# Performance work log

Hardware: AMD Instinct MI355X
Metric: run time of the kernel (lower is better)

Reference implementation:

```python
import jax, jax.numpy as jnp
from jax import lax
import numpy as np

B, S, H = 4, 4096, 1024
NH, HD, L = 8, 128, 64
EPS = 1e-8


def setup_inputs() -> dict:
    key = jax.random.key(0)
    ks = jax.random.split(key, 11)
    std = 0.02
    d = NH * HD
    return {
        "f_in": jax.random.normal(ks[0], (B, S, H), jnp.float32),
        "i_in": jax.random.normal(ks[1], (B, S, H), jnp.float32),
        "z_in": jax.random.normal(ks[2], (B, S, H), jnp.float32),
        "o_in": jax.random.normal(ks[3], (B, S, H), jnp.float32),
        "c0": jax.random.normal(ks[4], (B, NH, HD), jnp.float32),
        "h0": jax.random.normal(ks[5], (B, NH, HD), jnp.float32),
        "Wf": jax.random.normal(ks[6], (d, H), jnp.float32) * std,
        "bf": jnp.zeros((d,), jnp.float32),
        "Wi": jax.random.normal(ks[7], (d, H), jnp.float32) * std,
        "bi": jnp.zeros((d,), jnp.float32),
        "Wz": jax.random.normal(ks[8], (d, H), jnp.float32) * std,
        "bz": jnp.zeros((d,), jnp.float32),
        "Wo": jax.random.normal(ks[9], (d, H), jnp.float32) * std,
        "bo": jnp.zeros((d,), jnp.float32),
        "Wp": jax.random.normal(ks[10], (H, d), jnp.float32) * std,
        "bp": jnp.zeros((H,), jnp.float32),
    }


def _to_blocks(x):
    # (B,S,NH*HD) -> (n_blocks, B, NH, HD, L)
    nb = S // L
    return x.reshape(B, nb, L, NH, HD).transpose(1, 0, 3, 4, 2)


def reference(f_in, i_in, z_in, o_in, c0, h0, Wf, bf, Wi, bi, Wz, bz, Wo, bo, Wp, bp):
    fx = _to_blocks(f_in @ Wf.T + bf)
    ix = _to_blocks(i_in @ Wi.T + bi)
    zx = _to_blocks(z_in @ Wz.T + bz)
    ox = _to_blocks(o_in @ Wo.T + bo)

    f = jax.nn.sigmoid(fx + 1.0)            # (nb,B,NH,HD,L)
    o = jax.nn.sigmoid(ox)
    upd = jax.nn.sigmoid(ix) * jnp.tanh(zx)

    k = jnp.arange(L)[:, None]
    l = jnp.arange(L + 1)[None, :]
    ones_mask = l >= k + 1                   # set to 1 before cumulative log-prod
    zeros_mask = l >= k + 2                  # strictly-future entries zeroed

    def block_step(c, blk):
        fb, ub, ob = blk                     # each (B,NH,HD,L)
        cf = jnp.concatenate(
            [fb, jnp.ones(fb.shape[:3] + (1,), fb.dtype)], axis=3)  # (B,NH,HD,L+1)
        Fm = jnp.broadcast_to(cf[:, :, :, None, :], fb.shape[:3] + (L, L + 1))
        Fm = jnp.where(ones_mask, 1.0, Fm)
        # reverse cumulative product in log space (matches torch eps trick)
        Fm = jnp.exp(jnp.flip(jnp.cumsum(jnp.flip(jnp.log(Fm + EPS), -1), -1), -1)) - EPS
        Fm = jnp.where(zeros_mask, 0.0, Fm)  # (B,NH,HD,L,L+1)
        u = jnp.concatenate([c[..., None], ub], axis=3)  # (B,NH,HD,L+1)
        cs = jnp.einsum('bhdkl,bhdl->bhdk', Fm, u)       # (B,NH,HD,L)
        hs = ob * jnp.tanh(cs)
        return cs[..., -1], hs

    last_c, hs = lax.scan(block_step, c0, (f, upd, o))   # hs: (nb,B,NH,HD,L)
    last_h = hs[-1][..., -1]
    y = hs.transpose(1, 0, 4, 2, 3).reshape(B, S, NH * HD)
    y = y @ Wp.T + bp                                    # (B,S,H)
    return y, last_c, last_h
```

## Files before the change

kernel.cpp:

```cpp
#include <hip/hip_runtime.h>
#include <hip/hip_bf16.h>
#include <type_traits>

#define GATE_ELEMS 16777216ull
#define W_ELEMS    1048576ull

typedef float f32x4 __attribute__((ext_vector_type(4)));
typedef short s16x8 __attribute__((ext_vector_type(8)));
typedef unsigned short u16;

__device__ __forceinline__ u16 f2bf(float f) {
  union { float f; unsigned u; } v; v.f = f;
  unsigned r = v.u + 0x7fffu + ((v.u >> 16) & 1u);
  return (u16)(r >> 16);
}
__device__ __forceinline__ float bf2f(u16 u) {
  union { unsigned u; float f; } v; v.u = ((unsigned)u) << 16;
  return v.f;
}
__device__ __forceinline__ float sigmoidf_(float x) {
  return 1.0f / (1.0f + __expf(-x));
}
__device__ __forceinline__ float tanhf_(float x) {
  x = fminf(fmaxf(x, -15.f), 15.f);
  const float e = __expf(2.f * x);
  return (e - 1.f) / (e + 1.f);
}

__device__ __forceinline__ void load_lds16(const u16* g, u16* l) {
  __builtin_amdgcn_global_load_lds(
      (const __attribute__((address_space(1))) unsigned int*)g,
      (__attribute__((address_space(3))) unsigned int*)l, 16, 0, 0);
}

__global__ void cvt_x_kernel(const float* __restrict__ x0, const float* __restrict__ x1,
                             const float* __restrict__ x2, const float* __restrict__ x3,
                             u16* __restrict__ dst) {
  const float* src = (blockIdx.y == 0) ? x0 : (blockIdx.y == 1) ? x1
                   : (blockIdx.y == 2) ? x2 : x3;
  u16* d = dst + (size_t)blockIdx.y * GATE_ELEMS;
  const size_t i = ((size_t)blockIdx.x * 256 + threadIdx.x) * 8;
  const float4 a = *reinterpret_cast<const float4*>(src + i);
  const float4 b = *reinterpret_cast<const float4*>(src + i + 4);
  ushort4 lo = make_ushort4(f2bf(a.x), f2bf(a.y), f2bf(a.z), f2bf(a.w));
  ushort4 hi = make_ushort4(f2bf(b.x), f2bf(b.y), f2bf(b.z), f2bf(b.w));
  *reinterpret_cast<ushort4*>(d + i)     = lo;
  *reinterpret_cast<ushort4*>(d + i + 4) = hi;
}

__global__ void cvt_w_kernel(const float* __restrict__ w0, const float* __restrict__ w1,
                             const float* __restrict__ w2, const float* __restrict__ w3,
                             const float* __restrict__ w4, u16* __restrict__ dst) {
  const float* src = (blockIdx.y == 0) ? w0 : (blockIdx.y == 1) ? w1
                   : (blockIdx.y == 2) ? w2 : (blockIdx.y == 3) ? w3 : w4;
  u16* d = dst + (size_t)blockIdx.y * W_ELEMS;
  const size_t i = ((size_t)blockIdx.x * 256 + threadIdx.x) * 8;
  const float4 a = *reinterpret_cast<const float4*>(src + i);
  const float4 b = *reinterpret_cast<const float4*>(src + i + 4);
  ushort4 lo = make_ushort4(f2bf(a.x), f2bf(a.y), f2bf(a.z), f2bf(a.w));
  ushort4 hi = make_ushort4(f2bf(b.x), f2bf(b.y), f2bf(b.z), f2bf(b.w));
  *reinterpret_cast<ushort4*>(d + i)     = lo;
  *reinterpret_cast<ushort4*>(d + i + 4) = hi;
}

template <typename OT>
__global__ __launch_bounds__(256, 3)
void gemm_bt_bf16(const u16* __restrict__ A, const u16* __restrict__ B,
                  const float* __restrict__ bias, OT* __restrict__ C,
                  int M, int N, int K) {
  __shared__ __align__(16) u16 As[128 * 32];
  __shared__ __align__(16) u16 Bs[128 * 32];
  const int tid  = threadIdx.x;
  const int lane = tid & 63;
  const int wave = tid >> 6;
  const int wr = wave >> 1;
  const int wc = wave & 1;

  const int cpx = gridDim.x >> 3;
  int bid = blockIdx.x;
  bid = (bid & 7) * cpx + (bid >> 3);
  const int nbx = N >> 7;
  const int m0 = (bid / nbx) * 128;
  const int n0 = (bid % nbx) * 128;

  f32x4 acc[4][4];
#pragma unroll
  for (int i = 0; i < 4; ++i)
#pragma unroll
    for (int j = 0; j < 4; ++j)
      acc[i][j] = (f32x4){0.f, 0.f, 0.f, 0.f};

  const int frow = lane & 15;
  const int kq   = lane >> 4;
  const int krow = kq * 8;

  const int lrow = lane >> 2;
  const int lcol = (lane & 3) * 8;

  for (int kt = 0; kt < K; kt += 32) {
#pragma unroll
    for (int i = 0; i < 2; ++i) {
      const int rb = (i * 4 + wave) * 16;
      load_lds16(A + (size_t)(m0 + rb + lrow) * K + kt + lcol, &As[rb * 32]);
      load_lds16(B + (size_t)(n0 + rb + lrow) * K + kt + lcol, &Bs[rb * 32]);
    }
    __syncthreads();

    s16x8 afr[4], bfr[4];
#pragma unroll
    for (int mf = 0; mf < 4; ++mf)
      afr[mf] = *reinterpret_cast<const s16x8*>(&As[(wr * 64 + mf * 16 + frow) * 32 + krow]);
#pragma unroll
    for (int nf = 0; nf < 4; ++nf)
      bfr[nf] = *reinterpret_cast<const s16x8*>(&Bs[(wc * 64 + nf * 16 + frow) * 32 + krow]);
#pragma unroll
    for (int mf = 0; mf < 4; ++mf)
#pragma unroll
      for (int nf = 0; nf < 4; ++nf)
        acc[mf][nf] = __builtin_amdgcn_mfma_f32_16x16x32_bf16(afr[mf], bfr[nf], acc[mf][nf], 0, 0, 0);
    __syncthreads();
  }

#pragma unroll
  for (int nf = 0; nf < 4; ++nf) {
    const int col = n0 + wc * 64 + nf * 16 + frow;
    const float bv = bias[col];
#pragma unroll
    for (int mf = 0; mf < 4; ++mf) {
      const int rbase = m0 + wr * 64 + mf * 16 + kq * 4;
#pragma unroll
      for (int r = 0; r < 4; ++r) {
        const float v = acc[mf][nf][r] + bv;
        if constexpr (std::is_same<OT, float>::value)
          C[(size_t)(rbase + r) * N + col] = v;
        else
          C[(size_t)(rbase + r) * N + col] = f2bf(v);
      }
    }
  }
}

__global__ void scan_pass1(const u16* __restrict__ fx, const u16* __restrict__ ix,
                           const u16* __restrict__ zx,
                           float* __restrict__ P, float* __restrict__ cl) {
  const int t  = blockIdx.x * 256 + threadIdx.x;
  const int jg = (t & 255) * 4;
  const int q  = (t >> 8) & 63;
  const int b  = t >> 14;
  const size_t base = ((size_t)(b * 4096 + q * 64)) * 1024 + jg;
  float Pp[4] = {1.f, 1.f, 1.f, 1.f};
  float c[4]  = {0.f, 0.f, 0.f, 0.f};
  for (int s = 0; s < 64; ++s) {
    const size_t o = base + (size_t)s * 1024;
    const ushort4 fv = *reinterpret_cast<const ushort4*>(fx + o);
    const ushort4 iv = *reinterpret_cast<const ushort4*>(ix + o);
    const ushort4 zv = *reinterpret_cast<const ushort4*>(zx + o);
    const u16* fp = (const u16*)&fv;
    const u16* ip = (const u16*)&iv;
    const u16* zp = (const u16*)&zv;
#pragma unroll
    for (int k = 0; k < 4; ++k) {
      const float f = sigmoidf_(bf2f(fp[k]) + 1.f);
      const float u = sigmoidf_(bf2f(ip[k])) * tanhf_(bf2f(zp[k]));
      Pp[k] *= f;
      c[k] = f * c[k] + u;
    }
  }
  const int sidx = q * 4096 + b * 1024 + jg;
  *reinterpret_cast<float4*>(P + sidx)  = make_float4(Pp[0], Pp[1], Pp[2], Pp[3]);
  *reinterpret_cast<float4*>(cl + sidx) = make_float4(c[0], c[1], c[2], c[3]);
}

__global__ void scan_pass2(const float* __restrict__ P, const float* __restrict__ cl,
                           const float* __restrict__ c0, float* __restrict__ cin,
                           float* __restrict__ lastc) {
  const int idx = blockIdx.x * 256 + threadIdx.x;
  float carry = c0[idx];
#pragma unroll
  for (int q = 0; q < 64; ++q) {
    const int s = q * 4096 + idx;
    cin[s] = carry;
    carry = fmaf(P[s], carry, cl[s]);
  }
  lastc[idx] = carry;
}

__global__ void scan_pass3(const u16* __restrict__ fx, const u16* __restrict__ ix,
                           const u16* __restrict__ zx, const u16* __restrict__ ox,
                           const float* __restrict__ cin,
                           u16* __restrict__ h, float* __restrict__ lasth) {
  const int t  = blockIdx.x * 256 + threadIdx.x;
  const int jg = (t & 255) * 4;
  const int q  = (t >> 8) & 63;
  const int b  = t >> 14;
  const size_t base = ((size_t)(b * 4096 + q * 64)) * 1024 + jg;
  const float4 ci = *reinterpret_cast<const float4*>(cin + q * 4096 + b * 1024 + jg);
  float c[4]  = {ci.x, ci.y, ci.z, ci.w};
  float hv[4] = {0.f, 0.f, 0.f, 0.f};
  for (int s = 0; s < 64; ++s) {
    const size_t o = base + (size_t)s * 1024;
    const ushort4 fv = *reinterpret_cast<const ushort4*>(fx + o);
    const ushort4 iv = *reinterpret_cast<const ushort4*>(ix + o);
    const ushort4 zv = *reinterpret_cast<const ushort4*>(zx + o);
    const ushort4 ov = *reinterpret_cast<const ushort4*>(ox + o);
    const u16* fp = (const u16*)&fv;
    const u16* ip = (const u16*)&iv;
    const u16* zp = (const u16*)&zv;
    const u16* op = (const u16*)&ov;
    ushort4 hw;
    u16* hp = (u16*)&hw;
#pragma unroll
    for (int k = 0; k < 4; ++k) {
      const float f = sigmoidf_(bf2f(fp[k]) + 1.f);
      const float u = sigmoidf_(bf2f(ip[k])) * tanhf_(bf2f(zp[k]));
      c[k] = f * c[k] + u;
      hv[k] = sigmoidf_(bf2f(op[k])) * tanhf_(c[k]);
      hp[k] = f2bf(hv[k]);
    }
    *reinterpret_cast<ushort4*>(h + o) = hw;
  }
  if (q == 63)
    *reinterpret_cast<float4*>(lasth + b * 1024 + jg) =
        make_float4(hv[0], hv[1], hv[2], hv[3]);
}

extern "C" void kernel_launch(void* const* d_in, const int* in_sizes, int n_in,
                              void* d_out, int out_size, void* d_ws, size_t ws_size,
                              hipStream_t stream) {
  const float* xin[4]  = {(const float*)d_in[0], (const float*)d_in[1],
                          (const float*)d_in[2], (const float*)d_in[3]};
  const float* c0      = (const float*)d_in[4];
  const float* W[5]    = {(const float*)d_in[6], (const float*)d_in[8],
                          (const float*)d_in[10], (const float*)d_in[12],
                          (const float*)d_in[14]};
  const float* bias[5] = {(const float*)d_in[7], (const float*)d_in[9],
                          (const float*)d_in[11], (const float*)d_in[13],
                          (const float*)d_in[15]};
  float* out = (float*)d_out;

  u16* xbf = (u16*)d_ws;
  u16* wbf = xbf + 4 * GATE_ELEMS;
  float* Pbuf   = (float*)(wbf + 5 * W_ELEMS);
  float* clbuf  = Pbuf + 262144;
  float* cinbuf = clbuf + 262144;

  u16* gp[4];
  gp[0] = (u16*)d_out;
  gp[1] = xbf;
  gp[2] = xbf + GATE_ELEMS;
  gp[3] = xbf + 2 * GATE_ELEMS;
  u16* h = xbf + 3 * GATE_ELEMS;

  cvt_x_kernel<<<dim3(8192, 4), 256, 0, stream>>>(xin[0], xin[1], xin[2], xin[3], xbf);
  cvt_w_kernel<<<dim3(512, 5), 256, 0, stream>>>(W[0], W[1], W[2], W[3], W[4], wbf);

  const dim3 gg(1024, 1, 1);
  for (int g = 0; g < 4; ++g)
    gemm_bt_bf16<u16><<<gg, 256, 0, stream>>>(
        xbf + (size_t)g * GATE_ELEMS, wbf + (size_t)g * W_ELEMS, bias[g],
        gp[g], 16384, 1024, 1024);

  scan_pass1<<<256, 256, 0, stream>>>(gp[0], gp[1], gp[2], Pbuf, clbuf);
  scan_pass2<<<16, 256, 0, stream>>>(Pbuf, clbuf, c0, cinbuf, out + GATE_ELEMS);
  scan_pass3<<<256, 256, 0, stream>>>(gp[0], gp[1], gp[2], gp[3], cinbuf, h,
                                      out + GATE_ELEMS + 4096);

  gemm_bt_bf16<float><<<gg, 256, 0, stream>>>(h, wbf + 4 * W_ELEMS, bias[4],
                                              out, 16384, 1024, 1024);
}
```

Measured before the change: 671.1 us.

## Replace GEMM with 256x256-tile, 4-stage async-LDS pipelined bf16 kernel

Replaces the 128x128 single-buffered GEMM with a 256x256 tile kernel using 512 threads and a four-slot LDS ring buffer (128 KB dynamic shared memory). Global-to-LDS loads for tile k+3 are issued while MFMAs run on tile k, with explicit vmcnt waits, barriers and setprio to overlap memory with compute. The aim is to hide load latency and raise operand reuse per block. The x-conversion kernel also handles 16 elements per thread with 16-byte stores. Risks are lower occupancy from the large LDS footprint and fragile hand-tuned waitcnt logic.

```diff
diff --git a/kernel.cpp b/kernel.cpp
--- a/kernel.cpp
+++ b/kernel.cpp
@@ -39,13 +39,18 @@
   const float* src = (blockIdx.y == 0) ? x0 : (blockIdx.y == 1) ? x1
                    : (blockIdx.y == 2) ? x2 : x3;
   u16* d = dst + (size_t)blockIdx.y * GATE_ELEMS;
-  const size_t i = ((size_t)blockIdx.x * 256 + threadIdx.x) * 8;
-  const float4 a = *reinterpret_cast<const float4*>(src + i);
-  const float4 b = *reinterpret_cast<const float4*>(src + i + 4);
-  ushort4 lo = make_ushort4(f2bf(a.x), f2bf(a.y), f2bf(a.z), f2bf(a.w));
-  ushort4 hi = make_ushort4(f2bf(b.x), f2bf(b.y), f2bf(b.z), f2bf(b.w));
-  *reinterpret_cast<ushort4*>(d + i)     = lo;
-  *reinterpret_cast<ushort4*>(d + i + 4) = hi;
+  const size_t i = ((size_t)blockIdx.x * 256 + threadIdx.x) * 16;
+#pragma unroll
+  for (int half = 0; half < 2; ++half) {
+    const float4 a = *reinterpret_cast<const float4*>(src + i + half * 8);
+    const float4 b = *reinterpret_cast<const float4*>(src + i + half * 8 + 4);
+    s16x8 w;
+    w[0] = (short)f2bf(a.x); w[1] = (short)f2bf(a.y);
+    w[2] = (short)f2bf(a.z); w[3] = (short)f2bf(a.w);
+    w[4] = (short)f2bf(b.x); w[5] = (short)f2bf(b.y);
+    w[6] = (short)f2bf(b.z); w[7] = (short)f2bf(b.w);
+    *reinterpret_cast<s16x8*>(d + i + half * 8) = w;
+  }
 }
 
 __global__ void cvt_w_kernel(const float* __restrict__ w0, const float* __restrict__ w1,
@@ -57,84 +62,154 @@
   const size_t i = ((size_t)blockIdx.x * 256 + threadIdx.x) * 8;
   const float4 a = *reinterpret_cast<const float4*>(src + i);
   const float4 b = *reinterpret_cast<const float4*>(src + i + 4);
-  ushort4 lo = make_ushort4(f2bf(a.x), f2bf(a.y), f2bf(a.z), f2bf(a.w));
-  ushort4 hi = make_ushort4(f2bf(b.x), f2bf(b.y), f2bf(b.z), f2bf(b.w));
-  *reinterpret_cast<ushort4*>(d + i)     = lo;
-  *reinterpret_cast<ushort4*>(d + i + 4) = hi;
+  s16x8 w;
+  w[0] = (short)f2bf(a.x); w[1] = (short)f2bf(a.y);
+  w[2] = (short)f2bf(a.z); w[3] = (short)f2bf(a.w);
+  w[4] = (short)f2bf(b.x); w[5] = (short)f2bf(b.y);
+  w[6] = (short)f2bf(b.z); w[7] = (short)f2bf(b.w);
+  *reinterpret_cast<s16x8*>(d + i) = w;
+}
+
+__device__ __forceinline__ void stage_half(
+    const u16* __restrict__ A, const u16* __restrict__ B,
+    int m0, int n0, int kt, int hp, u16* lds, int tid) {
+  const u16* mat = (hp < 2) ? A : B;
+  const int gr0 = ((hp < 2) ? m0 : n0) + (hp & 1) * 128;
+  const int o   = tid * 16;
+  const int row = o >> 6;
+  const int col = (o & 63) >> 1;
+  const int slot = ((kt & 3) * 4 + hp) * 4096;
+  load_lds16(mat + (size_t)(gr0 + row) * 1024 + kt * 32 + col,
+             lds + slot + (tid >> 6) * 512);
 }
 
 template <typename OT>
-__global__ __launch_bounds__(256, 3)
-void gemm_bt_bf16(const u16* __restrict__ A, const u16* __restrict__ B,
-                  const float* __restrict__ bias, OT* __restrict__ C,
-                  int M, int N, int K) {
-  __shared__ __align__(16) u16 As[128 * 32];
-  __shared__ __align__(16) u16 Bs[128 * 32];
+__global__ __launch_bounds__(512, 2)
+void gemm_256(const u16* __restrict__ A, const u16* __restrict__ B,
+              const float* __restrict__ bias, OT* __restrict__ C) {
+  extern __shared__ u16 lds[];
   const int tid  = threadIdx.x;
   const int lane = tid & 63;
   const int wave = tid >> 6;
-  const int wr = wave >> 1;
-  const int wc = wave & 1;
-
-  const int cpx = gridDim.x >> 3;
+  const int wm = wave >> 2;
+  const int wn = wave & 3;
+  const int frow = lane & 15;
+  const int kq   = lane >> 4;
+
   int bid = blockIdx.x;
-  bid = (bid & 7) * cpx + (bid >> 3);
-  const int nbx = N >> 7;
-  const int m0 = (bid / nbx) * 128;
-  const int n0 = (bid % nbx) * 128;
-
-  f32x4 acc[4][4];
-#pragma unroll
-  for (int i = 0; i < 4; ++i)
+  bid = (bid & 7) * 32 + (bid >> 3);
+  const int m0 = (bid >> 2) * 256;
+  const int n0 = (bid & 3) * 256;
+
+  f32x4 acc[8][4];
+#pragma unroll
+  for (int i = 0; i < 8; ++i)
 #pragma unroll
     for (int j = 0; j < 4; ++j)
       acc[i][j] = (f32x4){0.f, 0.f, 0.f, 0.f};
 
-  const int frow = lane & 15;
-  const int kq   = lane >> 4;
-  const int krow = kq * 8;
-
-  const int lrow = lane >> 2;
-  const int lcol = (lane & 3) * 8;
-
-  for (int kt = 0; kt < K; kt += 32) {
-#pragma unroll
-    for (int i = 0; i < 2; ++i) {
-      const int rb = (i * 4 + wave) * 16;
-      load_lds16(A + (size_t)(m0 + rb + lrow) * K + kt + lcol, &As[rb * 32]);
-      load_lds16(B + (size_t)(n0 + rb + lrow) * K + kt + lcol, &Bs[rb * 32]);
-    }
-    __syncthreads();
-
-    s16x8 afr[4], bfr[4];
-#pragma unroll
-    for (int mf = 0; mf < 4; ++mf)
-      afr[mf] = *reinterpret_cast<const s16x8*>(&As[(wr * 64 + mf * 16 + frow) * 32 + krow]);
-#pragma unroll
-    for (int nf = 0; nf < 4; ++nf)
-      bfr[nf] = *reinterpret_cast<const s16x8*>(&Bs[(wc * 64 + nf * 16 + frow) * 32 + krow]);
-#pragma unroll
-    for (int mf = 0; mf < 4; ++mf)
-#pragma unroll
-      for (int nf = 0; nf < 4; ++nf)
-        acc[mf][nf] = __builtin_amdgcn_mfma_f32_16x16x32_bf16(afr[mf], bfr[nf], acc[mf][nf], 0, 0, 0);
-    __syncthreads();
+#pragma unroll
+  for (int k = 0; k < 3; ++k)
+#pragma unroll
+    for (int hp = 0; hp < 4; ++hp)
+      stage_half(A, B, m0, n0, k, hp, lds, tid);
+  asm volatile("s_waitcnt vmcnt(8)" ::: "memory");
+  __builtin_amdgcn_s_barrier();
+
+  const int rb = (wn & 1) * 64;
+
+#pragma unroll 4
+  for (int kt = 0; kt < 32; ++kt) {
+    const int slotbase = (kt & 3) * 4;
+    const u16* Ar = lds + (slotbase + wm) * 4096;
+    const u16* Br = lds + (slotbase + 2 + (wn >> 1)) * 4096;
+
+    s16x8 a0 = *reinterpret_cast<const s16x8*>(&Ar[(0 * 16 + frow) * 32 + kq * 8]);
+    s16x8 a1 = *reinterpret_cast<const s16x8*>(&Ar[(1 * 16 + frow) * 32 + kq * 8]);
+    s16x8 a2 = *reinterpret_cast<const s16x8*>(&Ar[(2 * 16 + frow) * 32 + kq * 8]);
+    s16x8 a3 = *reinterpret_cast<const s16x8*>(&Ar[(3 * 16 + frow) * 32 + kq * 8]);
+    s16x8 b0 = *reinterpret_cast<const s16x8*>(&Br[(rb + 0 * 16 + frow) * 32 + kq * 8]);
+    s16x8 b1 = *reinterpret_cast<const s16x8*>(&Br[(rb + 1 * 16 + frow) * 32 + kq * 8]);
+    s16x8 b2 = *reinterpret_cast<const s16x8*>(&Br[(rb + 2 * 16 + frow) * 32 + kq * 8]);
+    s16x8 b3 = *reinterpret_cast<const s16x8*>(&Br[(rb + 3 * 16 + frow) * 32 + kq * 8]);
+    if (kt <= 28) {
+      stage_half(A, B, m0, n0, kt + 3, 0, lds, tid);
+      stage_half(A, B, m0, n0, kt + 3, 1, lds, tid);
+    }
+    __builtin_amdgcn_s_barrier();
+    asm volatile("s_waitcnt lgkmcnt(0)" ::: "memory");
+    __builtin_amdgcn_sched_barrier(0);
+    __builtin_amdgcn_s_setprio(1);
+    acc[0][0] = __builtin_amdgcn_mfma_f32_16x16x32_bf16(a0, b0, acc[0][0], 0, 0, 0);
+    acc[0][1] = __builtin_amdgcn_mfma_f32_16x16x32_bf16(a0, b1, acc[0][1], 0, 0, 0);
+    acc[0][2] = __builtin_amdgcn_mfma_f32_16x16x32_bf16(a0, b2, acc[0][2], 0, 0, 0);
+    acc[0][3] = __builtin_amdgcn_mfma_f32_16x16x32_bf16(a0, b3, acc[0][3], 0, 0, 0);
+    acc[1][0] = __builtin_amdgcn_mfma_f32_16x16x32_bf16(a1, b0, acc[1][0], 0, 0, 0);
+    acc[1][1] = __builtin_amdgcn_mfma_f32_16x16x32_bf16(a1, b1, acc[1][1], 0, 0, 0);
+    acc[1][2] = __builtin_amdgcn_mfma_f32_16x16x32_bf16(a1, b2, acc[1][2], 0, 0, 0);
+    acc[1][3] = __builtin_amdgcn_mfma_f32_16x16x32_bf16(a1, b3, acc[1][3], 0, 0, 0);
+    acc[2][0] = __builtin_amdgcn_mfma_f32_16x16x32_bf16(a2, b0, acc[2][0], 0, 0, 0);
+    acc[2][1] = __builtin_amdgcn_mfma_f32_16x16x32_bf16(a2, b1, acc[2][1], 0, 0, 0);
+    acc[2][2] = __builtin_amdgcn_mfma_f32_16x16x32_bf16(a2, b2, acc[2][2], 0, 0, 0);
+    acc[2][3] = __builtin_amdgcn_mfma_f32_16x16x32_bf16(a2, b3, acc[2][3], 0, 0, 0);
+    acc[3][0] = __builtin_amdgcn_mfma_f32_16x16x32_bf16(a3, b0, acc[3][0], 0, 0, 0);
+    acc[3][1] = __builtin_amdgcn_mfma_f32_16x16x32_bf16(a3, b1, acc[3][1], 0, 0, 0);
+    acc[3][2] = __builtin_amdgcn_mfma_f32_16x16x32_bf16(a3, b2, acc[3][2], 0, 0, 0);
+    acc[3][3] = __builtin_amdgcn_mfma_f32_16x16x32_bf16(a3, b3, acc[3][3], 0, 0, 0);
+    __builtin_amdgcn_s_setprio(0);
+    __builtin_amdgcn_sched_barrier(0);
+    __builtin_amdgcn_s_barrier();
+
+    a0 = *reinterpret_cast<const s16x8*>(&Ar[(4 * 16 + frow) * 32 + kq * 8]);
+    a1 = *reinterpret_cast<const s16x8*>(&Ar[(5 * 16 + frow) * 32 + kq * 8]);
+    a2 = *reinterpret_cast<const s16x8*>(&Ar[(6 * 16 + frow) * 32 + kq * 8]);
+    a3 = *reinterpret_cast<const s16x8*>(&Ar[(7 * 16 + frow) * 32 + kq * 8]);
+    if (kt <= 28) {
+      stage_half(A, B, m0, n0, kt + 3, 2, lds, tid);
+      stage_half(A, B, m0, n0, kt + 3, 3, lds, tid);
+    }
+    __builtin_amdgcn_s_barrier();
+    asm volatile("s_waitcnt lgkmcnt(0)" ::: "memory");
+    __builtin_amdgcn_sched_barrier(0);
+    __builtin_amdgcn_s_setprio(1);
+    acc[4][0] = __builtin_amdgcn_mfma_f32_16x16x32_bf16(a0, b0, acc[4][0], 0, 0, 0);
+    acc[4][1] = __builtin_amdgcn_mfma_f32_16x16x32_bf16(a0, b1, acc[4][1], 0, 0, 0);
+    acc[4][2] = __builtin_amdgcn_mfma_f32_16x16x32_bf16(a0, b2, acc[4][2], 0, 0, 0);
+    acc[4][3] = __builtin_amdgcn_mfma_f32_16x16x32_bf16(a0, b3, acc[4][3], 0, 0, 0);
+    acc[5][0] = __builtin_amdgcn_mfma_f32_16x16x32_bf16(a1, b0, acc[5][0], 0, 0, 0);
+    acc[5][1] = __builtin_amdgcn_mfma_f32_16x16x32_bf16(a1, b1, acc[5][1], 0, 0, 0);
+    acc[5][2] = __builtin_amdgcn_mfma_f32_16x16x32_bf16(a1, b2, acc[5][2], 0, 0, 0);
+    acc[5][3] = __builtin_amdgcn_mfma_f32_16x16x32_bf16(a1, b3, acc[5][3], 0, 0, 0);
+    acc[6][0] = __builtin_amdgcn_mfma_f32_16x16x32_bf16(a2, b0, acc[6][0], 0, 0, 0);
+    acc[6][1] = __builtin_amdgcn_mfma_f32_16x16x32_bf16(a2, b1, acc[6][1], 0, 0, 0);
+    acc[6][2] = __builtin_amdgcn_mfma_f32_16x16x32_bf16(a2, b2, acc[6][2], 0, 0, 0);
+    acc[6][3] = __builtin_amdgcn_mfma_f32_16x16x32_bf16(a2, b3, acc[6][3], 0, 0, 0);
+    acc[7][0] = __builtin_amdgcn_mfma_f32_16x16x32_bf16(a3, b0, acc[7][0], 0, 0, 0);
+    acc[7][1] = __builtin_amdgcn_mfma_f32_16x16x32_bf16(a3, b1, acc[7][1], 0, 0, 0);
+    acc[7][2] = __builtin_amdgcn_mfma_f32_16x16x32_bf16(a3, b2, acc[7][2], 0, 0, 0);
+    acc[7][3] = __builtin_amdgcn_mfma_f32_16x16x32_bf16(a3, b3, acc[7][3], 0, 0, 0);
+    __builtin_amdgcn_s_setprio(0);
+    __builtin_amdgcn_sched_barrier(0);
+    if (kt <= 28)      asm volatile("s_waitcnt vmcnt(8)" ::: "memory");
+    else if (kt == 29) asm volatile("s_waitcnt vmcnt(4)" ::: "memory");
+    else if (kt == 30) asm volatile("s_waitcnt vmcnt(0)" ::: "memory");
+    __builtin_amdgcn_s_barrier();
   }
 
 #pragma unroll
   for (int nf = 0; nf < 4; ++nf) {
-    const int col = n0 + wc * 64 + nf * 16 + frow;
+    const int col = n0 + wn * 64 + nf * 16 + frow;
     const float bv = bias[col];
 #pragma unroll
-    for (int mf = 0; mf < 4; ++mf) {
-      const int rbase = m0 + wr * 64 + mf * 16 + kq * 4;
+    for (int mf = 0; mf < 8; ++mf) {
+      const int rbase = m0 + wm * 128 + mf * 16 + kq * 4;
 #pragma unroll
       for (int r = 0; r < 4; ++r) {
         const float v = acc[mf][nf][r] + bv;
         if constexpr (std::is_same<OT, float>::value)
-          C[(size_t)(rbase + r) * N + col] = v;
+          C[(size_t)(rbase + r) * 1024 + col] = v;
         else
-          C[(size_t)(rbase + r) * N + col] = f2bf(v);
+          C[(size_t)(rbase + r) * 1024 + col] = f2bf(v);
       }
     }
   }
@@ -238,6 +313,11 @@
                           (const float*)d_in[15]};
   float* out = (float*)d_out;
 
+  (void)hipFuncSetAttribute((const void*)gemm_256<u16>,
+                            hipFuncAttributeMaxDynamicSharedMemorySize, 131072);
+  (void)hipFuncSetAttribute((const void*)gemm_256<float>,
+                            hipFuncAttributeMaxDynamicSharedMemorySize, 131072);
+
   u16* xbf = (u16*)d_ws;
   u16* wbf = xbf + 4 * GATE_ELEMS;
   float* Pbuf   = (float*)(wbf + 5 * W_ELEMS);
@@ -251,20 +331,17 @@
   gp[3] = xbf + 2 * GATE_ELEMS;
   u16* h = xbf + 3 * GATE_ELEMS;
 
-  cvt_x_kernel<<<dim3(8192, 4), 256, 0, stream>>>(xin[0], xin[1], xin[2], xin[3], xbf);
+  cvt_x_kernel<<<dim3(4096, 4), 256, 0, stream>>>(xin[0], xin[1], xin[2], xin[3], xbf);
   cvt_w_kernel<<<dim3(512, 5), 256, 0, stream>>>(W[0], W[1], W[2], W[3], W[4], wbf);
 
-  const dim3 gg(1024, 1, 1);
   for (int g = 0; g < 4; ++g)
-    gemm_bt_bf16<u16><<<gg, 256, 0, stream>>>(
-        xbf + (size_t)g * GATE_ELEMS, wbf + (size_t)g * W_ELEMS, bias[g],
-        gp[g], 16384, 1024, 1024);
+    gemm_256<u16><<<256, 512, 131072, stream>>>(
+        xbf + (size_t)g * GATE_ELEMS, wbf + (size_t)g * W_ELEMS, bias[g], gp[g]);
 
   scan_pass1<<<256, 256, 0, stream>>>(gp[0], gp[1], gp[2], Pbuf, clbuf);
   scan_pass2<<<16, 256, 0, stream>>>(Pbuf, clbuf, c0, cinbuf, out + GATE_ELEMS);
   scan_pass3<<<256, 256, 0, stream>>>(gp[0], gp[1], gp[2], gp[3], cinbuf, h,
                                       out + GATE_ELEMS + 4096);
 
-  gemm_bt_bf16<float><<<gg, 256, 0, stream>>>(h, wbf + 4 * W_ELEMS, bias[4],
-                                              out, 16384, 1024, 1024);
-}
+  gemm_256<float><<<256, 512, 131072, stream>>>(h, wbf + 4 * W_ELEMS, bias[4], out);
+}
```

Measured after the change: 648.9 us. -3.3%, faster.

## Double-buffer GEMM with swizzled 64-wide K tiles and merge conversion kernels

Applied to the files above, without the earlier changes.

The GEMM now uses a K tile of 64 with two LDS buffers, so the next tile loads while the current one is computed, and it needs one barrier per step instead of two. LDS rows are XOR-swizzled to avoid bank conflicts. The two fp32-to-bf16 conversion kernels become one grid-stride kernel that writes 16-byte stores. The cost is 64KB of dynamic LDS per block and occupancy lowered to 2 blocks, and the shapes are hardcoded to 1024.

```diff
diff --git a/kernel.cpp b/kernel.cpp
--- a/kernel.cpp
+++ b/kernel.cpp
@@ -33,55 +33,69 @@
       (__attribute__((address_space(3))) unsigned int*)l, 16, 0, 0);
 }
 
-__global__ void cvt_x_kernel(const float* __restrict__ x0, const float* __restrict__ x1,
-                             const float* __restrict__ x2, const float* __restrict__ x3,
-                             u16* __restrict__ dst) {
-  const float* src = (blockIdx.y == 0) ? x0 : (blockIdx.y == 1) ? x1
-                   : (blockIdx.y == 2) ? x2 : x3;
-  u16* d = dst + (size_t)blockIdx.y * GATE_ELEMS;
-  const size_t i = ((size_t)blockIdx.x * 256 + threadIdx.x) * 8;
-  const float4 a = *reinterpret_cast<const float4*>(src + i);
-  const float4 b = *reinterpret_cast<const float4*>(src + i + 4);
-  ushort4 lo = make_ushort4(f2bf(a.x), f2bf(a.y), f2bf(a.z), f2bf(a.w));
-  ushort4 hi = make_ushort4(f2bf(b.x), f2bf(b.y), f2bf(b.z), f2bf(b.w));
-  *reinterpret_cast<ushort4*>(d + i)     = lo;
-  *reinterpret_cast<ushort4*>(d + i + 4) = hi;
-}
-
-__global__ void cvt_w_kernel(const float* __restrict__ w0, const float* __restrict__ w1,
-                             const float* __restrict__ w2, const float* __restrict__ w3,
-                             const float* __restrict__ w4, u16* __restrict__ dst) {
-  const float* src = (blockIdx.y == 0) ? w0 : (blockIdx.y == 1) ? w1
-                   : (blockIdx.y == 2) ? w2 : (blockIdx.y == 3) ? w3 : w4;
-  u16* d = dst + (size_t)blockIdx.y * W_ELEMS;
-  const size_t i = ((size_t)blockIdx.x * 256 + threadIdx.x) * 8;
-  const float4 a = *reinterpret_cast<const float4*>(src + i);
-  const float4 b = *reinterpret_cast<const float4*>(src + i + 4);
-  ushort4 lo = make_ushort4(f2bf(a.x), f2bf(a.y), f2bf(a.z), f2bf(a.w));
-  ushort4 hi = make_ushort4(f2bf(b.x), f2bf(b.y), f2bf(b.z), f2bf(b.w));
-  *reinterpret_cast<ushort4*>(d + i)     = lo;
-  *reinterpret_cast<ushort4*>(d + i + 4) = hi;
+#define XCHUNKS 8388608u
+#define WCHUNKS 655360u
+__global__ void cvt_all(const float* __restrict__ x0, const float* __restrict__ x1,
+                        const float* __restrict__ x2, const float* __restrict__ x3,
+                        const float* __restrict__ w0, const float* __restrict__ w1,
+                        const float* __restrict__ w2, const float* __restrict__ w3,
+                        const float* __restrict__ w4,
+                        u16* __restrict__ xdst, u16* __restrict__ wdst) {
+  const unsigned total = XCHUNKS + WCHUNKS;
+  for (unsigned i = blockIdx.x * 256 + threadIdx.x; i < total; i += 2048 * 256) {
+    const float* s; u16* d; size_t loc;
+    if (i < XCHUNKS) {
+      const int w = i >> 21;
+      loc = (size_t)(i & 2097151u) * 8;
+      s = (w == 0) ? x0 : (w == 1) ? x1 : (w == 2) ? x2 : x3;
+      d = xdst + (size_t)w * GATE_ELEMS;
+    } else {
+      const unsigned j = i - XCHUNKS;
+      const int w = j >> 17;
+      loc = (size_t)(j & 131071u) * 8;
+      s = (w == 0) ? w0 : (w == 1) ? w1 : (w == 2) ? w2 : (w == 3) ? w3 : w4;
+      d = wdst + (size_t)w * W_ELEMS;
+    }
+    const float4 a = *reinterpret_cast<const float4*>(s + loc);
+    const float4 b = *reinterpret_cast<const float4*>(s + loc + 4);
+    s16x8 wv;
+    wv[0] = (short)f2bf(a.x); wv[1] = (short)f2bf(a.y);
+    wv[2] = (short)f2bf(a.z); wv[3] = (short)f2bf(a.w);
+    wv[4] = (short)f2bf(b.x); wv[5] = (short)f2bf(b.y);
+    wv[6] = (short)f2bf(b.z); wv[7] = (short)f2bf(b.w);
+    *reinterpret_cast<s16x8*>(d + loc) = wv;
+  }
+}
+
+__device__ __forceinline__ void stage_mat(const u16* __restrict__ M, int R0, int kt,
+                                          u16* ldsbase, int tid) {
+#pragma unroll
+  for (int l = 0; l < 4; ++l) {
+    const int T  = l * 256 + tid;
+    const int r  = T >> 3;
+    const int sl = (T & 7) ^ (r & 7);
+    load_lds16(M + (size_t)(R0 + r) * 1024 + kt + sl * 8,
+               ldsbase + (T & ~63) * 8);
+  }
 }
 
 template <typename OT>
-__global__ __launch_bounds__(256, 3)
-void gemm_bt_bf16(const u16* __restrict__ A, const u16* __restrict__ B,
-                  const float* __restrict__ bias, OT* __restrict__ C,
-                  int M, int N, int K) {
-  __shared__ __align__(16) u16 As[128 * 32];
-  __shared__ __align__(16) u16 Bs[128 * 32];
+__global__ __launch_bounds__(256, 2)
+void gemm_bt128(const u16* __restrict__ A, const u16* __restrict__ Bm,
+                const float* __restrict__ bias, OT* __restrict__ C) {
+  extern __shared__ u16 lds[];
   const int tid  = threadIdx.x;
   const int lane = tid & 63;
   const int wave = tid >> 6;
   const int wr = wave >> 1;
   const int wc = wave & 1;
-
-  const int cpx = gridDim.x >> 3;
+  const int frow = lane & 15;
+  const int kq   = lane >> 4;
+
   int bid = blockIdx.x;
-  bid = (bid & 7) * cpx + (bid >> 3);
-  const int nbx = N >> 7;
-  const int m0 = (bid / nbx) * 128;
-  const int n0 = (bid % nbx) * 128;
+  bid = (bid & 7) * 128 + (bid >> 3);
+  const int m0 = (bid >> 3) * 128;
+  const int n0 = (bid & 7) * 128;
 
   f32x4 acc[4][4];
 #pragma unroll
@@ -90,35 +104,43 @@
     for (int j = 0; j < 4; ++j)
       acc[i][j] = (f32x4){0.f, 0.f, 0.f, 0.f};
 
-  const int frow = lane & 15;
-  const int kq   = lane >> 4;
-  const int krow = kq * 8;
-
-  const int lrow = lane >> 2;
-  const int lcol = (lane & 3) * 8;
-
-  for (int kt = 0; kt < K; kt += 32) {
-#pragma unroll
-    for (int i = 0; i < 2; ++i) {
-      const int rb = (i * 4 + wave) * 16;
-      load_lds16(A + (size_t)(m0 + rb + lrow) * K + kt + lcol, &As[rb * 32]);
-      load_lds16(B + (size_t)(n0 + rb + lrow) * K + kt + lcol, &Bs[rb * 32]);
+  stage_mat(A,  m0, 0, lds,        tid);
+  stage_mat(Bm, n0, 0, lds + 8192, tid);
+  __syncthreads();
+
+  int cur = 0;
+#pragma unroll 2
+  for (int t = 0; t < 16; ++t) {
+    if (t < 15) {
+      u16* nb = lds + (cur ^ 1) * 16384;
+      stage_mat(A,  m0, (t + 1) * 64, nb,        tid);
+      stage_mat(Bm, n0, (t + 1) * 64, nb + 8192, tid);
+    }
+    const u16* Ab = lds + cur * 16384;
+    const u16* Bb = Ab + 8192;
+#pragma unroll
+    for (int kk = 0; kk < 2; ++kk) {
+      s16x8 a[4], b[4];
+#pragma unroll
+      for (int mf = 0; mf < 4; ++mf) {
+        const int r  = wr * 64 + mf * 16 + frow;
+        const int ps = (kk * 4 + kq) ^ (r & 7);
+        a[mf] = *reinterpret_cast<const s16x8*>(&Ab[r * 64 + ps * 8]);
+      }
+#pragma unroll
+      for (int nf = 0; nf < 4; ++nf) {
+        const int r  = wc * 64 + nf * 16 + frow;
+        const int ps = (kk * 4 + kq) ^ (r & 7);
+        b[nf] = *reinterpret_cast<const s16x8*>(&Bb[r * 64 + ps * 8]);
+      }
+#pragma unroll
+      for (int mf = 0; mf < 4; ++mf)
+#pragma unroll
+        for (int nf = 0; nf < 4; ++nf)
+          acc[mf][nf] = __builtin_amdgcn_mfma_f32_16x16x32_bf16(a[mf], b[nf], acc[mf][nf], 0, 0, 0);
     }
     __syncthreads();
-
-    s16x8 afr[4], bfr[4];
-#pragma unroll
-    for (int mf = 0; mf < 4; ++mf)
-      afr[mf] = *reinterpret_cast<const s16x8*>(&As[(wr * 64 + mf * 16 + frow) * 32 + krow]);
-#pragma unroll
-    for (int nf = 0; nf < 4; ++nf)
-      bfr[nf] = *reinterpret_cast<const s16x8*>(&Bs[(wc * 64 + nf * 16 + frow) * 32 + krow]);
-#pragma unroll
-    for (int mf = 0; mf < 4; ++mf)
-#pragma unroll
-      for (int nf = 0; nf < 4; ++nf)
-        acc[mf][nf] = __builtin_amdgcn_mfma_f32_16x16x32_bf16(afr[mf], bfr[nf], acc[mf][nf], 0, 0, 0);
-    __syncthreads();
+    cur ^= 1;
   }
 
 #pragma unroll
@@ -132,9 +154,9 @@
       for (int r = 0; r < 4; ++r) {
         const float v = acc[mf][nf][r] + bv;
         if constexpr (std::is_same<OT, float>::value)
-          C[(size_t)(rbase + r) * N + col] = v;
+          C[(size_t)(rbase + r) * 1024 + col] = v;
         else
-          C[(size_t)(rbase + r) * N + col] = f2bf(v);
+          C[(size_t)(rbase + r) * 1024 + col] = f2bf(v);
       }
     }
   }
@@ -238,6 +260,11 @@
                           (const float*)d_in[15]};
   float* out = (float*)d_out;
 
+  (void)hipFuncSetAttribute((const void*)gemm_bt128<u16>,
+                            hipFuncAttributeMaxDynamicSharedMemorySize, 65536);
+  (void)hipFuncSetAttribute((const void*)gemm_bt128<float>,
+                            hipFuncAttributeMaxDynamicSharedMemorySize, 65536);
+
   u16* xbf = (u16*)d_ws;
   u16* wbf = xbf + 4 * GATE_ELEMS;
   float* Pbuf   = (float*)(wbf + 5 * W_ELEMS);
@@ -251,20 +278,17 @@
   gp[3] = xbf + 2 * GATE_ELEMS;
   u16* h = xbf + 3 * GATE_ELEMS;
 
-  cvt_x_kernel<<<dim3(8192, 4), 256, 0, stream>>>(xin[0], xin[1], xin[2], xin[3], xbf);
-  cvt_w_kernel<<<dim3(512, 5), 256, 0, stream>>>(W[0], W[1], W[2], W[3], W[4], wbf);
-
-  const dim3 gg(1024, 1, 1);
+  cvt_all<<<2048, 256, 0, stream>>>(xin[0], xin[1], xin[2], xin[3],
+                                    W[0], W[1], W[2], W[3], W[4], xbf, wbf);
+
   for (int g = 0; g < 4; ++g)
-    gemm_bt_bf16<u16><<<gg, 256, 0, stream>>>(
-        xbf + (size_t)g * GATE_ELEMS, wbf + (size_t)g * W_ELEMS, bias[g],
-        gp[g], 16384, 1024, 1024);
+    gemm_bt128<u16><<<1024, 256, 65536, stream>>>(
+        xbf + (size_t)g * GATE_ELEMS, wbf + (size_t)g * W_ELEMS, bias[g], gp[g]);
 
   scan_pass1<<<256, 256, 0, stream>>>(gp[0], gp[1], gp[2], Pbuf, clbuf);
   scan_pass2<<<16, 256, 0, stream>>>(Pbuf, clbuf, c0, cinbuf, out + GATE_ELEMS);
   scan_pass3<<<256, 256, 0, stream>>>(gp[0], gp[1], gp[2], gp[3], cinbuf, h,
                                       out + GATE_ELEMS + 4096);
 
-  gemm_bt_bf16<float><<<gg, 256, 0, stream>>>(h, wbf + 4 * W_ELEMS, bias[4],
-                                              out, 16384, 1024, 1024);
-}
+  gemm_bt128<float><<<1024, 256, 65536, stream>>>(h, wbf + 4 * W_ELEMS, bias[4], out);
+}
```

Measured after the change: 677.6 us. Within noise of the previous version (+1.0%).
